# Optimization experiments

Measured on AMD Instinct MI355X. Metric: run time of the kernel, lower is better.

Reference implementation:

```python
import jax, jax.numpy as jnp
from jax import lax
import numpy as np

B, N, WID = 4096, 16, 64


def setup_inputs() -> dict:
    key = jax.random.key(0)
    ks = jax.random.split(key, 10)
    def nrm(k, shape, fan):
        return (jax.random.normal(k, shape) / np.float32(np.sqrt(fan))).astype(jnp.float32)
    x = 2.0 * jax.random.randint(ks[0], (B, N, N), 0, 2).astype(jnp.float32) - 1.0  # spins +/-1
    return {
        "x": x,
        "Wx": nrm(ks[1], (1, 2), 2),          # intermediate_x: Linear(2,1,bias=False)
        "Wh": nrm(ks[2], (WID, 2 * WID), 2 * WID),   # intermediate_h
        "Wh2": nrm(ks[3], (WID, 2 * WID), 2 * WID),  # intermediate_h2
        "Wih": nrm(ks[4], (4 * WID, 2), 2),   # LSTMCell weight_ih
        "Whh": nrm(ks[5], (4 * WID, WID), WID),  # LSTMCell weight_hh
        "bih": nrm(ks[6], (4 * WID,), WID),
        "bhh": nrm(ks[7], (4 * WID,), WID),
        "Wfc": nrm(ks[8], (2, WID), WID),     # fc1
        "bfc": nrm(ks[9], (2,), WID),
    }


def _log_prob(x, Wx, Wh, Wh2, Wih, Whh, bih, bhh, Wfc, bfc):
    Bn, n, _ = x.shape
    Wd = Whh.shape[1]
    dt = x.dtype

    # zigzag traversal: even rows left->right, odd rows right->left.
    # perm maps traversal position t -> column index; involutive (identity or reversal).
    perms = jnp.stack([jnp.arange(n) if i % 2 == 0 else jnp.arange(n)[::-1]
                       for i in range(n)])  # [n, n]
    x_rows = jnp.transpose(x, (1, 0, 2))                                  # [n, B, n]
    x_up_rows = jnp.concatenate([jnp.zeros((1, Bn, n), dt), x_rows[:-1]], 0)  # [n, B, n]

    Wh_p, Wh_u = Wh[:, :Wd], Wh[:, Wd:]
    Wh2_p, Wh2_u = Wh2[:, :Wd], Wh2[:, Wd:]

    def cell(carry, xs):
        h_prev, c_prev = carry          # [B, W] each (in-row previous cell, zeros at row start)
        x_prev, x_up, h_up, c_up = xs   # [B], [B], [B,W], [B,W]
        # slot 1 = previous cell along traversal, slot 2 = cell above
        x_inter = x_prev * Wx[0, 0] + x_up * Wx[0, 1]                     # [B]
        h_inter = h_prev @ Wh_p.T + h_up @ Wh_u.T                          # [B, W]
        c_inter = c_prev @ Wh2_p.T + c_up @ Wh2_u.T                        # [B, W]
        xh = (x_inter + 1.0) * 0.5
        emb = jnp.stack([xh, 1.0 - xh], axis=-1)                           # [B, 2]
        gates = emb @ Wih.T + bih + h_inter @ Whh.T + bhh                  # [B, 4W]
        ig, fg, gg, og = jnp.split(gates, 4, axis=-1)
        c_new = jax.nn.sigmoid(fg) * c_inter + jax.nn.sigmoid(ig) * jnp.tanh(gg)
        h_new = jax.nn.sigmoid(og) * jnp.tanh(c_new)
        y = jax.nn.log_softmax(h_new @ Wfc.T + bfc, axis=-1)               # [B, 2]
        return (h_new, c_new), (h_new, c_new, y)

    def row_step(carry, xs):
        h_row, c_row = carry            # [B, n, W] states of previous row (column order)
        x_row, x_up_row, perm = xs
        x_trav = x_row[:, perm]                                            # [B, n]
        x_prev_trav = jnp.concatenate([jnp.zeros((Bn, 1), dt), x_trav[:, :-1]], 1)
        x_up_trav = x_up_row[:, perm]
        h_up_trav = jnp.transpose(h_row[:, perm], (1, 0, 2))               # [n, B, W]
        c_up_trav = jnp.transpose(c_row[:, perm], (1, 0, 2))
        init = (jnp.zeros((Bn, Wd), dt), jnp.zeros((Bn, Wd), dt))
        _, (h_t, c_t, y_t) = lax.scan(
            cell, init, (x_prev_trav.T, x_up_trav.T, h_up_trav, c_up_trav))
        # traversal order -> column order (perm is its own inverse)
        h_col = jnp.transpose(h_t[perm], (1, 0, 2))                        # [B, n, W]
        c_col = jnp.transpose(c_t[perm], (1, 0, 2))
        y_col = y_t[perm]                                                  # [n, B, 2]
        return (h_col, c_col), y_col

    init = (jnp.zeros((Bn, n, Wd), dt), jnp.zeros((Bn, n, Wd), dt))
    _, ys = lax.scan(row_step, init, (x_rows, x_up_rows, perms))           # [n, n, B, 2]
    y = jnp.transpose(ys, (2, 0, 1, 3))                                    # [B, n, n, 2]

    mask = (1.0 + x) * 0.5
    lp = y[..., 0] * mask + y[..., 1] * (1.0 - mask)                       # [B, n, n]
    # final correction: samples with exactly one up spin
    aa = mask.sum((1, 2))
    rec = aa == 1
    jc = 0 if n % 2 == 0 else n - 1  # last visited cell of the zigzag
    factor = jnp.where(rec, 1.0 - mask[:, n - 1, jc], jnp.ones((), dt))
    lp = lp.at[:, n - 1, jc].multiply(factor)
    return lp.sum((1, 2))


def reference(x, Wx, Wh, Wh2, Wih, Whh, bih, bhh, Wfc, bfc):
    return _log_prob(x, Wx, Wh, Wh2, Wih, Whh, bih, bhh, Wfc, bfc)
```

## Files before the change

kernel.cpp:

```cpp
#include <hip/hip_runtime.h>

typedef __bf16 bf16x8 __attribute__((ext_vector_type(8)));
typedef float f32x4 __attribute__((ext_vector_type(4)));

#define MFMA(a,b,c) __builtin_amdgcn_mfma_f32_16x16x32_bf16((a),(b),(c),0,0,0)

__device__ __forceinline__ float rcp_(float x){ return __builtin_amdgcn_rcpf(x); }

#define L2E 1.4426950408889634f
#define LN2 0.6931471805599453f

__global__ __launch_bounds__(256) void prep_kernel(
    const float* __restrict__ Wh,  const float* __restrict__ Wh2,
    const float* __restrict__ Whh, const float* __restrict__ Wfc,
    const float* __restrict__ Wih, const float* __restrict__ bih,
    const float* __restrict__ bhh,
    char* __restrict__ tblc)
{
  const int idx = blockIdx.x*256 + threadIdx.x;
  if (idx < 512*14*8){
    const int e = idx & 7, f = (idx >> 3) % 14, t = (idx >> 3) / 14;
    const int w = t >> 6, lane = t & 63, l16 = lane & 15;
    const int g8 = ((lane >> 4) & 3) * 8;
    const int hcol = w*8 + (l16 & 7), hi = l16 >> 3;
    float val;
    if (f < 8){
      const int half = (f >> 2) & 1;
      const int tile = (f >> 1) & 1;
      const int s    = f & 1;
      const int gate = tile*2 + hi;
      const int n = gate*64 + hcol;
      const int k = s*32 + g8 + e;
      float acc = 0.f;
      for (int j=0; j<64; ++j) acc += Whh[n*64 + j] * Wh[j*128 + half*64 + k];
      val = acc * ((gate == 2) ? 2.f*L2E : L2E);
    } else if (f < 12){
      const int s = f - 8;
      const int k = (s & 1)*32 + g8 + e;
      val = Wh2[hcol*128 + (s >> 1)*64 + k];
    } else {
      const int k = (f & 1)*32 + g8 + e;
      val = Wfc[k] - Wfc[64 + k];
    }
    *(__bf16*)(tblc + t*240 + f*16 + e*2) = (__bf16)val;
  } else if (idx < 512*14*8 + 512*4){
    const int j = idx - 512*14*8;
    const int t = j >> 2, q = j & 3;
    const int w = t >> 6, lane = t & 63, l16 = lane & 15, hi = l16 >> 3;
    const int tile = q >> 1, kind = q & 1;
    const int gate = tile*2 + hi;
    const int n = gate*64 + w*8 + (l16 & 7);
    const float sc = (gate == 2) ? 2.f*L2E : L2E;
    const float v = kind ? sc*(Wih[n*2] - Wih[n*2+1])
                         : sc*(bih[n] + bhh[n] + Wih[n*2+1]);
    *(float*)(tblc + t*240 + 224 + q*4) = v;
  }
}

__global__ __launch_bounds__(512,2) void lstm2d_kernel(
    const float* __restrict__ x,   const float* __restrict__ Wx,
    const float* __restrict__ bfc,
    const char* __restrict__ tblc,
    float* __restrict__ out)
{
  __shared__ __align__(16) __bf16 s_h[16*16*64];
  __shared__ __align__(16) __bf16 s_c[16*16*64];
  __shared__ __align__(16) float  s_xh[256*16];
  __shared__ __align__(16) float  s_d[256*16];
  __shared__ unsigned int s_msk[16*8];
  __shared__ float s_red[8*16];

  const int tid  = threadIdx.x;
  const int w    = tid >> 6;
  const int lane = tid & 63;
  const int l16  = lane & 15;
  const int g4   = lane >> 4;
  const int g8   = g4 * 8;
  const int hi   = l16 >> 3;
  const bool lo  = (hi == 0);

  const float wx0 = Wx[0], wx1 = Wx[1];
  const float bd  = bfc[0] - bfc[1];

  unsigned int* zh = (unsigned int*)s_h;
  unsigned int* zc = (unsigned int*)s_c;
  #pragma unroll
  for (int it=0; it<16; ++it){ zh[tid + it*512] = 0u; zc[tid + it*512] = 0u; }

  const float* xg = x + blockIdx.x * 4096;
  #pragma unroll
  for (int k=0; k<8; ++k){
    const int idx = tid + k*512;
    const int row = idx & 15, slot = idx >> 4;
    const int i = slot >> 4, t = slot & 15;
    const int c   = (i & 1) ? 15 - t : t;
    const int cpc = (i & 1) ? c + 1 : c - 1;
    const float xp = (t > 0) ? xg[row*256 + i*16 + cpc] : 0.f;
    const float xu = (i > 0) ? xg[row*256 + (i-1)*16 + c] : 0.f;
    s_xh[slot*16 + row] = (xp*wx0 + xu*wx1 + 1.f) * 0.5f;
  }
  if (tid < 128){
    const int row = tid >> 3, wd = tid & 7;
    unsigned int m = 0;
    for (int b=0; b<32; ++b){
      const int slot = wd*32 + b, i = slot >> 4, t = slot & 15;
      const int c = (i & 1) ? 15 - t : t;
      if (xg[row*256 + i*16 + c] > 0.f) m |= (1u << b);
    }
    s_msk[row*8 + wd] = m;
  }

  const char* tb = tblc + tid*240;
  bf16x8 g1T0[2], g1T1[2], g2T0[2], g2T1[2], cB[4], fcB[2];
  g1T0[0] = *(const bf16x8*)(tb +   0); g1T0[1] = *(const bf16x8*)(tb +  16);
  g1T1[0] = *(const bf16x8*)(tb +  32); g1T1[1] = *(const bf16x8*)(tb +  48);
  g2T0[0] = *(const bf16x8*)(tb +  64); g2T0[1] = *(const bf16x8*)(tb +  80);
  g2T1[0] = *(const bf16x8*)(tb +  96); g2T1[1] = *(const bf16x8*)(tb + 112);
  #pragma unroll
  for (int s=0; s<4; ++s) cB[s] = *(const bf16x8*)(tb + 128 + s*16);
  fcB[0] = *(const bf16x8*)(tb + 192); fcB[1] = *(const bf16x8*)(tb + 208);
  const float base0 = *(const float*)(tb + 224);
  const float dvec0 = *(const float*)(tb + 228);
  const float base1 = *(const float*)(tb + 232);
  const float dvec1 = *(const float*)(tb + 236);

  const int offA0 = l16*64 + ((     g8) ^ ((l16 & 7) << 3));
  const int offA1 = l16*64 + ((32 + g8) ^ ((l16 & 7) << 3));
  const int habs = w*8 + (l16 & 7);
  int stWa[2];
  #pragma unroll
  for (int e=0; e<2; ++e){
    const int R = g4*4 + 2*hi + e;
    stWa[e] = R*64 + (habs ^ ((R & 7) << 3));
  }
  const float C2 = -2.f*L2E;

  __syncthreads();

  f32x4 aT0u, aT1u, aCu;

  for (int i=0; i<16; ++i){
    const int dir = i & 1;
    const int slot0 = i*16;

    {
      const int bu = (dir ? 15 : 0) << 10;
      bf16x8 h0 = *(const bf16x8*)(s_h + bu + offA0);
      bf16x8 h1 = *(const bf16x8*)(s_h + bu + offA1);
      bf16x8 c0 = *(const bf16x8*)(s_c + bu + offA0);
      bf16x8 c1 = *(const bf16x8*)(s_c + bu + offA1);
      const float4 xh4 = *(const float4*)(s_xh + slot0*16 + g4*4);
      #pragma unroll
      for (int r=0;r<4;++r){
        const float xh = (&xh4.x)[r];
        aT0u[r] = base0 + xh*dvec0;
        aT1u[r] = base1 + xh*dvec1;
      }
      aT0u = MFMA(h0, g2T0[0], aT0u); aT0u = MFMA(h1, g2T0[1], aT0u);
      aT1u = MFMA(h0, g2T1[0], aT1u); aT1u = MFMA(h1, g2T1[1], aT1u);
      f32x4 z = {0.f,0.f,0.f,0.f};
      aCu = MFMA(c0, cB[2], z); aCu = MFMA(c1, cB[3], aCu);
      if (w == 0 && i > 0){
        f32x4 fz = {bd,bd,bd,bd};
        fz = MFMA(h0, fcB[0], fz);
        f32x4 aF = MFMA(h1, fcB[1], fz);
        if (l16 == 0){
          #pragma unroll
          for (int r=0;r<4;++r) s_d[(slot0-1)*16 + g4*4 + r] = aF[r];
        }
      }
    }

    for (int t=0; t<16; ++t){
      const int c    = dir ? 15 - t : t;
      const int slot = slot0 + t;

      f32x4 aT0 = aT0u, aT1 = aT1u, aC = aCu;
      if (t > 0){
        const int bp = (dir ? c + 1 : c - 1) << 10;
        bf16x8 a0 = *(const bf16x8*)(s_h + bp + offA0);
        bf16x8 a1 = *(const bf16x8*)(s_h + bp + offA1);
        bf16x8 q0 = *(const bf16x8*)(s_c + bp + offA0);
        bf16x8 q1 = *(const bf16x8*)(s_c + bp + offA1);
        aT0 = MFMA(a0, g1T0[0], aT0); aT0 = MFMA(a1, g1T0[1], aT0);
        aT1 = MFMA(a0, g1T1[0], aT1); aT1 = MFMA(a1, g1T1[1], aT1);
        aC  = MFMA(q0, cB[0], aC);    aC  = MFMA(q1, cB[1], aC);
        if (w == 0){
          f32x4 fz = {bd,bd,bd,bd};
          fz = MFMA(a0, fcB[0], fz);
          f32x4 aF = MFMA(a1, fcB[1], fz);
          if (l16 == 0){
            #pragma unroll
            for (int r=0;r<4;++r) s_d[(slot-1)*16 + g4*4 + r] = aF[r];
          }
        }
      }

      if (t < 15){
        const int bu = (dir ? 14 - t : t + 1) << 10;
        bf16x8 h0 = *(const bf16x8*)(s_h + bu + offA0);
        bf16x8 h1 = *(const bf16x8*)(s_h + bu + offA1);
        bf16x8 c0 = *(const bf16x8*)(s_c + bu + offA0);
        bf16x8 c1 = *(const bf16x8*)(s_c + bu + offA1);
        const float4 xh4 = *(const float4*)(s_xh + (slot+1)*16 + g4*4);
        #pragma unroll
        for (int r=0;r<4;++r){
          const float xh = (&xh4.x)[r];
          aT0u[r] = base0 + xh*dvec0;
          aT1u[r] = base1 + xh*dvec1;
        }
        aT0u = MFMA(h0, g2T0[0], aT0u); aT0u = MFMA(h1, g2T0[1], aT0u);
        aT1u = MFMA(h0, g2T1[0], aT1u); aT1u = MFMA(h1, g2T1[1], aT1u);
        f32x4 z = {0.f,0.f,0.f,0.f};
        aCu = MFMA(c0, cB[2], z); aCu = MFMA(c1, cB[3], aCu);
      }

      const int cb = c << 10;
      #pragma unroll
      for (int e=0; e<2; ++e){
        const float sendT0 = lo ? aT0[2+e] : aT0[e];
        const float sendT1 = lo ? aT1[2+e] : aT1[e];
        const float rT0 = __shfl_xor(sendT0, 8);
        const float rT1 = __shfl_xor(sendT1, 8);
        const float own0 = lo ? aT0[e] : aT0[2+e];
        const float own1 = lo ? aT1[e] : aT1[2+e];
        const float ig = lo ? own0 : rT0;
        const float fg = lo ? rT0  : own0;
        const float gg = lo ? own1 : rT1;
        const float og = lo ? rT1  : own1;
        const float cI = lo ? aC[e] : aC[2+e];
        const float si = rcp_(1.f + exp2f(-ig));
        const float sf = rcp_(1.f + exp2f(-fg));
        const float tg = 2.f * rcp_(1.f + exp2f(-gg)) - 1.f;
        const float cn = sf*cI + si*tg;
        const float so = rcp_(1.f + exp2f(-og));
        const float tc = 2.f * rcp_(1.f + exp2f(C2*cn)) - 1.f;
        const float hn = so * tc;
        s_h[cb + stWa[e]] = (__bf16)hn;
        s_c[cb + stWa[e]] = (__bf16)cn;
      }

      __syncthreads();
    }
  }

  if (w == 0){
    bf16x8 a0 = *(const bf16x8*)(s_h + offA0);
    bf16x8 a1 = *(const bf16x8*)(s_h + offA1);
    f32x4 fz = {bd,bd,bd,bd};
    fz = MFMA(a0, fcB[0], fz);
    f32x4 aF = MFMA(a1, fcB[1], fz);
    if (l16 == 0){
      #pragma unroll
      for (int r=0;r<4;++r) s_d[255*16 + g4*4 + r] = aF[r];
    }
  }
  __syncthreads();

  {
    const int row = tid & 15, grp = tid >> 4;
    float lpp = 0.f;
    #pragma unroll
    for (int e=0; e<8; ++e){
      const int slot = grp*8 + e;
      const float d = s_d[slot*16 + row];
      const int msk = (s_msk[row*8 + (slot >> 5)] >> (slot & 31)) & 1;
      const float zz = msk ? -d : d;
      lpp -= LN2 * log2f(1.f + exp2f(zz * L2E));
    }
    lpp += __shfl_xor(lpp, 16);
    lpp += __shfl_xor(lpp, 32);
    if (lane < 16) s_red[w*16 + lane] = lpp;
  }
  __syncthreads();
  if (tid < 16){
    const int row = tid;
    float lp = 0.f;
    #pragma unroll
    for (int ww=0; ww<8; ++ww) lp += s_red[ww*16 + row];
    int aa = 0;
    #pragma unroll
    for (int wd=0; wd<8; ++wd) aa += __popc(s_msk[row*8 + wd]);
    const int m255 = (s_msk[row*8 + 7] >> 31) & 1;
    if (aa == 1 && m255){
      const float d = s_d[255*16 + row];
      lp += LN2 * log2f(1.f + exp2f(-d * L2E));
    }
    out[blockIdx.x*16 + row] = lp;
  }
}

extern "C" void kernel_launch(void* const* d_in, const int* in_sizes, int n_in,
                              void* d_out, int out_size, void* d_ws, size_t ws_size,
                              hipStream_t stream) {
  const float* x   = (const float*)d_in[0];
  const float* Wx  = (const float*)d_in[1];
  const float* Wh  = (const float*)d_in[2];
  const float* Wh2 = (const float*)d_in[3];
  const float* Wih = (const float*)d_in[4];
  const float* Whh = (const float*)d_in[5];
  const float* bih = (const float*)d_in[6];
  const float* bhh = (const float*)d_in[7];
  const float* Wfc = (const float*)d_in[8];
  const float* bfc = (const float*)d_in[9];
  float* out = (float*)d_out;
  char* tbl = (char*)d_ws;

  prep_kernel<<<dim3(((512*14*8 + 512*4) + 255)/256), dim3(256), 0, stream>>>(
      Wh, Wh2, Whh, Wfc, Wih, bih, bhh, tbl);
  lstm2d_kernel<<<dim3(256), dim3(512), 0, stream>>>(x, Wx, bfc, tbl, out);
}
```

Before: 274.4 us.

## Restructure LSTM step: hoist LDS loads, merge gate reciprocals, rotate fc wave

Inside the 16-step row loop, all shared-memory loads for both the previous-cell and above-cell operands are now issued up front. The next-step above-cell MFMAs move after the gate nonlinearity, so load latency and MFMA work can overlap the transcendental math. The gate math is rewritten algebraically so the sigmoid and tanh reciprocals share fewer rcp calls. The fc-projection work rotates across waves instead of always landing on wave 0, and launch bounds drop to min 1 block per CU. The final reduction drops the shuffles in favour of a larger shared buffer, and uses fast __logf/__expf. The merged reciprocal form may lose precision or overflow when the exp terms are large.

Measured after the change: 254.9 us. -7.1%, faster.

```diff
diff --git a/kernel.cpp b/kernel.cpp
--- a/kernel.cpp
+++ b/kernel.cpp
@@ -8,7 +8,6 @@
 __device__ __forceinline__ float rcp_(float x){ return __builtin_amdgcn_rcpf(x); }
 
 #define L2E 1.4426950408889634f
-#define LN2 0.6931471805599453f
 
 __global__ __launch_bounds__(256) void prep_kernel(
     const float* __restrict__ Wh,  const float* __restrict__ Wh2,
@@ -57,7 +56,7 @@
   }
 }
 
-__global__ __launch_bounds__(512,2) void lstm2d_kernel(
+__global__ __launch_bounds__(512,1) void lstm2d_kernel(
     const float* __restrict__ x,   const float* __restrict__ Wx,
     const float* __restrict__ bfc,
     const char* __restrict__ tblc,
@@ -68,7 +67,7 @@
   __shared__ __align__(16) float  s_xh[256*16];
   __shared__ __align__(16) float  s_d[256*16];
   __shared__ unsigned int s_msk[16*8];
-  __shared__ float s_red[8*16];
+  __shared__ float s_red[512];
 
   const int tid  = threadIdx.x;
   const int w    = tid >> 6;
@@ -133,6 +132,7 @@
     const int R = g4*4 + 2*hi + e;
     stWa[e] = R*64 + (habs ^ ((R & 7) << 3));
   }
+  const int xhOff = g4*4;
   const float C2 = -2.f*L2E;
 
   __syncthreads();
@@ -149,7 +149,7 @@
       bf16x8 h1 = *(const bf16x8*)(s_h + bu + offA1);
       bf16x8 c0 = *(const bf16x8*)(s_c + bu + offA0);
       bf16x8 c1 = *(const bf16x8*)(s_c + bu + offA1);
-      const float4 xh4 = *(const float4*)(s_xh + slot0*16 + g4*4);
+      const float4 xh4 = *(const float4*)(s_xh + slot0*16 + xhOff);
       #pragma unroll
       for (int r=0;r<4;++r){
         const float xh = (&xh4.x)[r];
@@ -160,7 +160,7 @@
       aT1u = MFMA(h0, g2T1[0], aT1u); aT1u = MFMA(h1, g2T1[1], aT1u);
       f32x4 z = {0.f,0.f,0.f,0.f};
       aCu = MFMA(c0, cB[2], z); aCu = MFMA(c1, cB[3], aCu);
-      if (w == 0 && i > 0){
+      if (i > 0 && w == 7){
         f32x4 fz = {bd,bd,bd,bd};
         fz = MFMA(h0, fcB[0], fz);
         f32x4 aF = MFMA(h1, fcB[1], fz);
@@ -171,21 +171,37 @@
       }
     }
 
+    #pragma unroll 4
     for (int t=0; t<16; ++t){
       const int c    = dir ? 15 - t : t;
       const int slot = slot0 + t;
-
-      f32x4 aT0 = aT0u, aT1 = aT1u, aC = aCu;
+      const int cb   = c << 10;
+
+      bf16x8 a0, a1, q0, q1;
       if (t > 0){
-        const int bp = (dir ? c + 1 : c - 1) << 10;
-        bf16x8 a0 = *(const bf16x8*)(s_h + bp + offA0);
-        bf16x8 a1 = *(const bf16x8*)(s_h + bp + offA1);
-        bf16x8 q0 = *(const bf16x8*)(s_c + bp + offA0);
-        bf16x8 q1 = *(const bf16x8*)(s_c + bp + offA1);
-        aT0 = MFMA(a0, g1T0[0], aT0); aT0 = MFMA(a1, g1T0[1], aT0);
-        aT1 = MFMA(a0, g1T1[0], aT1); aT1 = MFMA(a1, g1T1[1], aT1);
-        aC  = MFMA(q0, cB[0], aC);    aC  = MFMA(q1, cB[1], aC);
-        if (w == 0){
+        const int b = (dir ? c + 1 : c - 1) << 10;
+        a0 = *(const bf16x8*)(s_h + b + offA0);
+        a1 = *(const bf16x8*)(s_h + b + offA1);
+        q0 = *(const bf16x8*)(s_c + b + offA0);
+        q1 = *(const bf16x8*)(s_c + b + offA1);
+      }
+      bf16x8 au0, au1, cu0, cu1;
+      float4 xh4n;
+      if (t < 15){
+        const int bu = (dir ? 14 - t : t + 1) << 10;
+        au0 = *(const bf16x8*)(s_h + bu + offA0);
+        au1 = *(const bf16x8*)(s_h + bu + offA1);
+        cu0 = *(const bf16x8*)(s_c + bu + offA0);
+        cu1 = *(const bf16x8*)(s_c + bu + offA1);
+        xh4n = *(const float4*)(s_xh + (slot+1)*16 + xhOff);
+      }
+
+      f32x4 aT0, aT1, aC;
+      if (t > 0){
+        aT0 = MFMA(a0, g1T0[0], aT0u); aT0 = MFMA(a1, g1T0[1], aT0);
+        aT1 = MFMA(a0, g1T1[0], aT1u); aT1 = MFMA(a1, g1T1[1], aT1);
+        aC  = MFMA(q0, cB[0], aCu);    aC  = MFMA(q1, cB[1], aC);
+        if (w == ((t - 1) & 7)){
           f32x4 fz = {bd,bd,bd,bd};
           fz = MFMA(a0, fcB[0], fz);
           f32x4 aF = MFMA(a1, fcB[1], fz);
@@ -194,28 +210,10 @@
             for (int r=0;r<4;++r) s_d[(slot-1)*16 + g4*4 + r] = aF[r];
           }
         }
-      }
-
-      if (t < 15){
-        const int bu = (dir ? 14 - t : t + 1) << 10;
-        bf16x8 h0 = *(const bf16x8*)(s_h + bu + offA0);
-        bf16x8 h1 = *(const bf16x8*)(s_h + bu + offA1);
-        bf16x8 c0 = *(const bf16x8*)(s_c + bu + offA0);
-        bf16x8 c1 = *(const bf16x8*)(s_c + bu + offA1);
-        const float4 xh4 = *(const float4*)(s_xh + (slot+1)*16 + g4*4);
-        #pragma unroll
-        for (int r=0;r<4;++r){
-          const float xh = (&xh4.x)[r];
-          aT0u[r] = base0 + xh*dvec0;
-          aT1u[r] = base1 + xh*dvec1;
-        }
-        aT0u = MFMA(h0, g2T0[0], aT0u); aT0u = MFMA(h1, g2T0[1], aT0u);
-        aT1u = MFMA(h0, g2T1[0], aT1u); aT1u = MFMA(h1, g2T1[1], aT1u);
-        f32x4 z = {0.f,0.f,0.f,0.f};
-        aCu = MFMA(c0, cB[2], z); aCu = MFMA(c1, cB[3], aCu);
-      }
-
-      const int cb = c << 10;
+      } else {
+        aT0 = aT0u; aT1 = aT1u; aC = aCu;
+      }
+
       #pragma unroll
       for (int e=0; e<2; ++e){
         const float sendT0 = lo ? aT0[2+e] : aT0[e];
@@ -229,22 +227,38 @@
         const float gg = lo ? own1 : rT1;
         const float og = lo ? rT1  : own1;
         const float cI = lo ? aC[e] : aC[2+e];
-        const float si = rcp_(1.f + exp2f(-ig));
-        const float sf = rcp_(1.f + exp2f(-fg));
-        const float tg = 2.f * rcp_(1.f + exp2f(-gg)) - 1.f;
-        const float cn = sf*cI + si*tg;
-        const float so = rcp_(1.f + exp2f(-og));
-        const float tc = 2.f * rcp_(1.f + exp2f(C2*cn)) - 1.f;
-        const float hn = so * tc;
+        const float A = exp2f(-ig);
+        const float F = exp2f(-fg);
+        const float B = exp2f(-gg);
+        const float O = exp2f(-og);
+        const float a1_ = 1.f + A, f1 = 1.f + F, b1 = 1.f + B, o1 = 1.f + O;
+        const float pab = a1_ * b1;
+        const float num = fmaf(1.f - B, f1, cI * pab);
+        const float cn  = num * rcp_(pab * f1);
+        const float E   = exp2f(C2 * cn);
+        const float hn  = (1.f - E) * rcp_(o1 * (1.f + E));
         s_h[cb + stWa[e]] = (__bf16)hn;
         s_c[cb + stWa[e]] = (__bf16)cn;
       }
 
+      if (t < 15){
+        #pragma unroll
+        for (int r=0;r<4;++r){
+          const float xh = (&xh4n.x)[r];
+          aT0u[r] = base0 + xh*dvec0;
+          aT1u[r] = base1 + xh*dvec1;
+        }
+        aT0u = MFMA(au0, g2T0[0], aT0u); aT0u = MFMA(au1, g2T0[1], aT0u);
+        aT1u = MFMA(au0, g2T1[0], aT1u); aT1u = MFMA(au1, g2T1[1], aT1u);
+        f32x4 z = {0.f,0.f,0.f,0.f};
+        aCu = MFMA(cu0, cB[2], z); aCu = MFMA(cu1, cB[3], aCu);
+      }
+
       __syncthreads();
     }
   }
 
-  if (w == 0){
+  if (w == 7){
     bf16x8 a0 = *(const bf16x8*)(s_h + offA0);
     bf16x8 a1 = *(const bf16x8*)(s_h + offA1);
     f32x4 fz = {bd,bd,bd,bd};
@@ -266,25 +280,23 @@
       const float d = s_d[slot*16 + row];
       const int msk = (s_msk[row*8 + (slot >> 5)] >> (slot & 31)) & 1;
       const float zz = msk ? -d : d;
-      lpp -= LN2 * log2f(1.f + exp2f(zz * L2E));
-    }
-    lpp += __shfl_xor(lpp, 16);
-    lpp += __shfl_xor(lpp, 32);
-    if (lane < 16) s_red[w*16 + lane] = lpp;
+      lpp -= __logf(1.f + __expf(zz));
+    }
+    s_red[grp*16 + row] = lpp;
   }
   __syncthreads();
   if (tid < 16){
     const int row = tid;
     float lp = 0.f;
     #pragma unroll
-    for (int ww=0; ww<8; ++ww) lp += s_red[ww*16 + row];
+    for (int g=0; g<32; ++g) lp += s_red[g*16 + row];
     int aa = 0;
     #pragma unroll
     for (int wd=0; wd<8; ++wd) aa += __popc(s_msk[row*8 + wd]);
     const int m255 = (s_msk[row*8 + 7] >> 31) & 1;
     if (aa == 1 && m255){
       const float d = s_d[255*16 + row];
-      lp += LN2 * log2f(1.f + exp2f(-d * L2E));
+      lp += __logf(1.f + __expf(-d));
     }
     out[blockIdx.x*16 + row] = lp;
   }
@@ -306,7 +318,7 @@
   float* out = (float*)d_out;
   char* tbl = (char*)d_ws;
 
-  prep_kernel<<<dim3(((512*14*8 + 512*4) + 255)/256), dim3(256), 0, stream>>>(
+  prep_kernel<<<dim3(232), dim3(256), 0, stream>>>(
       Wh, Wh2, Whh, Wfc, Wih, bih, bhh, tbl);
   lstm2d_kernel<<<dim3(256), dim3(512), 0, stream>>>(x, Wx, bfc, tbl, out);
 }
```
